# Kernel tuning notes

Hardware: AMD Instinct MI355X
Metric: run time of the kernel (lower is better)

Reference implementation:

```python
import jax, jax.numpy as jnp
import numpy as np

ALPHA = 1.702
LIMIT = 7.0
TOP_K = 2
B, S, H, E, I = 2, 1024, 768, 8, 768


def setup_inputs() -> dict:
    key = jax.random.key(0)
    ks = jax.random.split(key, 7)
    scale = 0.02
    return {
        "hidden_states": jax.random.normal(ks[0], (B, S, H), dtype=jnp.float32),
        "Wr": jax.random.normal(ks[1], (H, E), dtype=jnp.float32) * scale,
        "br": jax.random.normal(ks[2], (E,), dtype=jnp.float32) * scale,
        "Wgu": jax.random.normal(ks[3], (E, H, 2 * I), dtype=jnp.float32) * scale,
        "bgu": jax.random.normal(ks[4], (E, 2 * I), dtype=jnp.float32) * scale,
        "Wd": jax.random.normal(ks[5], (E, I, H), dtype=jnp.float32) * scale,
        "bd": jax.random.normal(ks[6], (E, H), dtype=jnp.float32) * scale,
    }


def reference(hidden_states, Wr, br, Wgu, bgu, Wd, bd):
    # Router: top-K experts per token, softmax over the K selected logits
    logits = jnp.einsum("bsh,he->bse", hidden_states, Wr) + br
    topk_vals, topk_idx = jax.lax.top_k(logits, TOP_K)        # [B,S,K]
    router_scores = jax.nn.softmax(topk_vals, axis=-1)         # [B,S,K]

    # Dense-over-experts grouped GEMM (sparse_matmul reference: unselected
    # experts are computed but never read by the combine gather below).
    gu = jnp.einsum("bsh,ehf->bsef", hidden_states, Wgu) + bgu  # [B,S,E,2I]
    gu = jnp.minimum(gu, LIMIT)
    gate = gu[..., :I]
    up = jnp.maximum(gu[..., I:], -LIMIT)
    glu = gate * jax.nn.sigmoid(gate * ALPHA)
    activated = (up + 1.0) * glu                                # [B,S,E,I]

    down = jnp.einsum("bsei,eih->bseh", activated, Wd) + bd     # [B,S,E,H]

    # all_to_all_combine (num_devices=1): gather this token's K expert outputs
    sel = jnp.take_along_axis(down, topk_idx[..., None], axis=2)  # [B,S,K,H]
    output = jnp.sum(sel * router_scores[..., None], axis=2)      # [B,S,H]
    return output
```

## Files before the change

### kernel.cpp

```cpp
#include <hip/hip_runtime.h>
#include <hip/hip_bf16.h>
#include <cmath>

#define ALPHA 1.702f
#define LIMIT 7.0f

constexpr int B = 2, S = 1024, H = 768, E = 8, I = 768;
constexpr int T = B * S;
constexpr int TWO_I = 2 * I;
constexpr int CAP = T;
constexpr int NROWS = T * 2;

typedef __attribute__((ext_vector_type(8))) short short8;
typedef __attribute__((ext_vector_type(4))) float floatx4;

__device__ __forceinline__ unsigned short f2bf(float v) {
  __hip_bfloat16 h = __float2bfloat16(v);
  return *reinterpret_cast<unsigned short*>(&h);
}

__device__ __forceinline__ void g2l16(const void* g, void* l) {
  __builtin_amdgcn_global_load_lds(
      (const __attribute__((address_space(1))) void*)g,
      (__attribute__((address_space(3))) void*)l, 16, 0, 0);
}

__global__ __launch_bounds__(64) void router_kernel(
    const float* __restrict__ x, const float* __restrict__ Wr,
    const float* __restrict__ br, int* __restrict__ topk_idx,
    float* __restrict__ topk_w, unsigned short* __restrict__ xb,
    float* __restrict__ out) {
  int t = blockIdx.x;
  int lane = threadIdx.x;
  const float* xr = x + (size_t)t * H;

  float4 z4 = {0.f, 0.f, 0.f, 0.f};
#pragma unroll
  for (int j = 0; j < 3; j++)
    *(float4*)(out + (size_t)t * H + (size_t)(j * 64 + lane) * 4) = z4;

  float acc[E];
#pragma unroll
  for (int e = 0; e < E; e++) acc[e] = 0.0f;

#pragma unroll
  for (int it = 0; it < 3; it++) {
    int h4 = it * 64 + lane;
    float4 xv = *(const float4*)(xr + (size_t)h4 * 4);
    ushort4 xo;
    xo.x = f2bf(xv.x);
    xo.y = f2bf(xv.y);
    xo.z = f2bf(xv.z);
    xo.w = f2bf(xv.w);
    *(ushort4*)(xb + (size_t)t * H + (size_t)h4 * 4) = xo;
    const float* wrow = Wr + (size_t)h4 * 4 * E;
    float xs[4] = {xv.x, xv.y, xv.z, xv.w};
#pragma unroll
    for (int j = 0; j < 4; j++)
#pragma unroll
      for (int e = 0; e < E; e++) acc[e] += xs[j] * wrow[j * E + e];
  }
#pragma unroll
  for (int e = 0; e < E; e++) {
    float v = acc[e];
    for (int off = 32; off > 0; off >>= 1) v += __shfl_down(v, off, 64);
    acc[e] = v;
  }
  if (lane == 0) {
    float logits[E];
#pragma unroll
    for (int e = 0; e < E; e++) logits[e] = acc[e] + br[e];
    int i0 = 0;
    float v0 = logits[0];
#pragma unroll
    for (int e = 1; e < E; e++)
      if (logits[e] > v0) { v0 = logits[e]; i0 = e; }
    int i1 = -1;
    float v1 = -INFINITY;
#pragma unroll
    for (int e = 0; e < E; e++) {
      if (e == i0) continue;
      if (logits[e] > v1) { v1 = logits[e]; i1 = e; }
    }
    float s1 = __expf(v1 - v0);
    float denom = 1.0f + s1;
    topk_idx[t * 2 + 0] = i0;
    topk_idx[t * 2 + 1] = i1;
    topk_w[t * 2 + 0] = 1.0f / denom;
    topk_w[t * 2 + 1] = s1 / denom;
  }
}

__global__ __launch_bounds__(256) void transpose_all(
    const float* __restrict__ Wgu, const float* __restrict__ Wd,
    unsigned short* __restrict__ Wgt, unsigned short* __restrict__ Wdt,
    const int* __restrict__ topk_idx, const float* __restrict__ topk_w,
    int* __restrict__ e_cnt, int* __restrict__ row_token,
    float* __restrict__ row_w) {
  int z = blockIdx.z;
  int tid = threadIdx.x;

  if (z == 16) {
    if (blockIdx.x != 0 || blockIdx.y != 0) return;
    __shared__ int cur[E];
    if (tid < E) cur[tid] = 0;
    __syncthreads();
    for (int i = tid; i < NROWS; i += 256) {
      int e = topk_idx[i];
      int pos = atomicAdd(&cur[e], 1);
      row_token[e * CAP + pos] = i >> 1;
      row_w[e * CAP + pos] = topk_w[i];
    }
    __syncthreads();
    if (tid < E) e_cnt[tid] = cur[tid];
    return;
  }

  int which = z >> 3, e = z & 7;
  int N = which ? H : TWO_I;
  if (which && blockIdx.x >= (H / 64)) return;
  const float* in = which ? (Wd + (size_t)e * H * I)
                          : (Wgu + (size_t)e * H * TWO_I);
  unsigned short* out = which ? (Wdt + (size_t)e * H * I)
                              : (Wgt + (size_t)e * H * TWO_I);
  constexpr int K = 768;
  int n0 = blockIdx.x * 64, k0 = blockIdx.y * 64;

  __shared__ float tile[64][65];
  int jr = tid & 15, r0 = tid >> 4;
#pragma unroll
  for (int p = 0; p < 4; p++) {
    int k = r0 + p * 16;
    float4 v = *(const float4*)(in + (size_t)(k0 + k) * N + n0 + jr * 4);
    tile[k][jr * 4 + 0] = v.x;
    tile[k][jr * 4 + 1] = v.y;
    tile[k][jr * 4 + 2] = v.z;
    tile[k][jr * 4 + 3] = v.w;
  }
  __syncthreads();
#pragma unroll
  for (int p = 0; p < 4; p++) {
    int n = r0 + p * 16;
    ushort4 o;
    o.x = f2bf(tile[jr * 4 + 0][n]);
    o.y = f2bf(tile[jr * 4 + 1][n]);
    o.z = f2bf(tile[jr * 4 + 2][n]);
    o.w = f2bf(tile[jr * 4 + 3][n]);
    *(ushort4*)(out + (size_t)(n0 + n) * K + k0 + jr * 4) = o;
  }
}

__global__ __launch_bounds__(256) void gemm_gu_mfma(
    const unsigned short* __restrict__ xb, const unsigned short* __restrict__ Wgt,
    const float* __restrict__ bgu, const int* __restrict__ e_cnt,
    const int* __restrict__ row_token, unsigned short* __restrict__ act) {
  int e = blockIdx.z;
  int cnt = e_cnt[e];
  int m0 = blockIdx.y * 128;
  if (m0 >= cnt) return;
  int n0 = blockIdx.x * 64;
  int start = e * CAP;
  const unsigned short* Wg = Wgt + (size_t)e * TWO_I * H;
  const float* bias = bgu + (size_t)e * TWO_I;

  __shared__ short As[2][128 * 64];
  __shared__ short Bg[2][64 * 64];
  __shared__ short Bu[2][64 * 64];
  __shared__ int tok[128];

  int tid = threadIdx.x;
  if (tid < 128) {
    int m = m0 + tid;
    tok[tid] = row_token[start + ((m < cnt) ? m : (cnt - 1))];
  }
  __syncthreads();

  int lane = tid & 63;
  int wave = tid >> 6;
  int quad = lane >> 4;
  int lrow = lane & 15;
  int wm = (wave >> 1) * 64;
  int wn = (wave & 1) * 32;

  const unsigned short* gA[4];
  int oA[4];
#pragma unroll
  for (int r = 0; r < 4; r++) {
    int s = (wave * 4 + r) * 64 + lane;
    int row = s >> 3;
    int g = (s & 7) ^ (row & 7);
    gA[r] = xb + (size_t)tok[row] * H + g * 8;
    oA[r] = (wave * 4 + r) * 64 * 8;
  }
  const unsigned short *gBg[2], *gBu[2];
  int oB[2];
#pragma unroll
  for (int r = 0; r < 2; r++) {
    int s = (wave * 2 + r) * 64 + lane;
    int row = s >> 3;
    int g = (s & 7) ^ (row & 7);
    gBg[r] = Wg + (size_t)(n0 + row) * H + g * 8;
    gBu[r] = gBg[r] + (size_t)I * H;
    oB[r] = (wave * 2 + r) * 64 * 8;
  }

  float bgv[2], buv[2];
#pragma unroll
  for (int tj = 0; tj < 2; tj++) {
    int ncol = n0 + wn + tj * 16 + lrow;
    bgv[tj] = bias[ncol];
    buv[tj] = bias[I + ncol];
  }

  floatx4 accg[4][2], accu[4][2];
#pragma unroll
  for (int i = 0; i < 4; i++)
#pragma unroll
    for (int j = 0; j < 2; j++) {
      accg[i][j] = floatx4{0.f, 0.f, 0.f, 0.f};
      accu[i][j] = floatx4{0.f, 0.f, 0.f, 0.f};
    }

  __syncthreads();

#pragma unroll
  for (int r = 0; r < 4; r++) g2l16(gA[r], &As[0][oA[r]]);
#pragma unroll
  for (int r = 0; r < 2; r++) {
    g2l16(gBg[r], &Bg[0][oB[r]]);
    g2l16(gBu[r], &Bu[0][oB[r]]);
  }

  constexpr int NK = H / 64;
  for (int i = 0; i < NK; i++) {
    int cb = i & 1;
    if (i + 1 < NK) {
      int nb = cb ^ 1;
      int k1 = (i + 1) * 64;
#pragma unroll
      for (int r = 0; r < 4; r++) g2l16(gA[r] + k1, &As[nb][oA[r]]);
#pragma unroll
      for (int r = 0; r < 2; r++) {
        g2l16(gBg[r] + k1, &Bg[nb][oB[r]]);
        g2l16(gBu[r] + k1, &Bu[nb][oB[r]]);
      }
      asm volatile("s_waitcnt vmcnt(8)" ::: "memory");
    } else {
      asm volatile("s_waitcnt vmcnt(0)" ::: "memory");
    }
    __builtin_amdgcn_s_barrier();

#pragma unroll
    for (int ks = 0; ks < 2; ks++) {
      int c = ks * 4 + quad;
      short8 a[4], bg[2], bu[2];
#pragma unroll
      for (int ti = 0; ti < 4; ti++) {
        int r = wm + ti * 16 + lrow;
        a[ti] = *(const short8*)(&As[cb][(r * 8 + (c ^ (r & 7))) * 8]);
      }
#pragma unroll
      for (int tj = 0; tj < 2; tj++) {
        int r = wn + tj * 16 + lrow;
        bg[tj] = *(const short8*)(&Bg[cb][(r * 8 + (c ^ (r & 7))) * 8]);
        bu[tj] = *(const short8*)(&Bu[cb][(r * 8 + (c ^ (r & 7))) * 8]);
      }
#pragma unroll
      for (int ti = 0; ti < 4; ti++)
#pragma unroll
        for (int tj = 0; tj < 2; tj++) {
          accg[ti][tj] = __builtin_amdgcn_mfma_f32_16x16x32_bf16(
              a[ti], bg[tj], accg[ti][tj], 0, 0, 0);
          accu[ti][tj] = __builtin_amdgcn_mfma_f32_16x16x32_bf16(
              a[ti], bu[tj], accu[ti][tj], 0, 0, 0);
        }
    }
    __builtin_amdgcn_s_barrier();
  }

#pragma unroll
  for (int ti = 0; ti < 4; ti++) {
#pragma unroll
    for (int tj = 0; tj < 2; tj++) {
      int ncol = n0 + wn + tj * 16 + lrow;
#pragma unroll
      for (int r = 0; r < 4; r++) {
        int m = m0 + wm + ti * 16 + quad * 4 + r;
        if (m < cnt) {
          float g = accg[ti][tj][r] + bgv[tj];
          float u = accu[ti][tj][r] + buv[tj];
          g = fminf(g, LIMIT);
          u = fmaxf(fminf(u, LIMIT), -LIMIT);
          float glu = g / (1.0f + __expf(-ALPHA * g));
          act[(size_t)(start + m) * I + ncol] = f2bf((u + 1.0f) * glu);
        }
      }
    }
  }
}

__global__ __launch_bounds__(256) void gemm_down_mfma(
    const unsigned short* __restrict__ act, const unsigned short* __restrict__ Wdt,
    const float* __restrict__ bd, const int* __restrict__ e_cnt,
    const int* __restrict__ row_token, const float* __restrict__ row_w,
    float* __restrict__ out) {
  int e = blockIdx.z;
  int cnt = e_cnt[e];
  int m0 = blockIdx.y * 128;
  if (m0 >= cnt) return;
  int n0 = blockIdx.x * 64;
  int start = e * CAP;
  const unsigned short* Wd = Wdt + (size_t)e * H * I;
  const float* bias = bd + (size_t)e * H;

  __shared__ short As[2][128 * 64];
  __shared__ short Bs[2][64 * 64];
  __shared__ int tok[128];
  __shared__ float wts[128];

  int tid = threadIdx.x;
  if (tid < 128) {
    int m = m0 + tid;
    int mm = (m < cnt) ? m : (cnt - 1);
    tok[tid] = row_token[start + mm];
    wts[tid] = row_w[start + mm];
  }
  __syncthreads();

  int lane = tid & 63;
  int wave = tid >> 6;
  int quad = lane >> 4;
  int lrow = lane & 15;
  int wm = (wave >> 1) * 64;
  int wn = (wave & 1) * 32;

  const unsigned short* gA[4];
  int oA[4];
#pragma unroll
  for (int r = 0; r < 4; r++) {
    int s = (wave * 4 + r) * 64 + lane;
    int row = s >> 3;
    int g = (s & 7) ^ (row & 7);
    int gm = m0 + row;
    int mm = (gm < cnt) ? gm : (cnt - 1);
    gA[r] = act + (size_t)(start + mm) * I + g * 8;
    oA[r] = (wave * 4 + r) * 64 * 8;
  }
  const unsigned short* gB[2];
  int oB[2];
#pragma unroll
  for (int r = 0; r < 2; r++) {
    int s = (wave * 2 + r) * 64 + lane;
    int row = s >> 3;
    int g = (s & 7) ^ (row & 7);
    gB[r] = Wd + (size_t)(n0 + row) * I + g * 8;
    oB[r] = (wave * 2 + r) * 64 * 8;
  }

  float bdv[2];
#pragma unroll
  for (int tj = 0; tj < 2; tj++) bdv[tj] = bias[n0 + wn + tj * 16 + lrow];

  floatx4 acc[4][2];
#pragma unroll
  for (int i = 0; i < 4; i++)
#pragma unroll
    for (int j = 0; j < 2; j++) acc[i][j] = floatx4{0.f, 0.f, 0.f, 0.f};

  __syncthreads();

#pragma unroll
  for (int r = 0; r < 4; r++) g2l16(gA[r], &As[0][oA[r]]);
#pragma unroll
  for (int r = 0; r < 2; r++) g2l16(gB[r], &Bs[0][oB[r]]);

  constexpr int NK = I / 64;
  for (int i = 0; i < NK; i++) {
    int cb = i & 1;
    if (i + 1 < NK) {
      int nb = cb ^ 1;
      int k1 = (i + 1) * 64;
#pragma unroll
      for (int r = 0; r < 4; r++) g2l16(gA[r] + k1, &As[nb][oA[r]]);
#pragma unroll
      for (int r = 0; r < 2; r++) g2l16(gB[r] + k1, &Bs[nb][oB[r]]);
      asm volatile("s_waitcnt vmcnt(6)" ::: "memory");
    } else {
      asm volatile("s_waitcnt vmcnt(0)" ::: "memory");
    }
    __builtin_amdgcn_s_barrier();

#pragma unroll
    for (int ks = 0; ks < 2; ks++) {
      int c = ks * 4 + quad;
      short8 a[4], b[2];
#pragma unroll
      for (int ti = 0; ti < 4; ti++) {
        int r = wm + ti * 16 + lrow;
        a[ti] = *(const short8*)(&As[cb][(r * 8 + (c ^ (r & 7))) * 8]);
      }
#pragma unroll
      for (int tj = 0; tj < 2; tj++) {
        int r = wn + tj * 16 + lrow;
        b[tj] = *(const short8*)(&Bs[cb][(r * 8 + (c ^ (r & 7))) * 8]);
      }
#pragma unroll
      for (int ti = 0; ti < 4; ti++)
#pragma unroll
        for (int tj = 0; tj < 2; tj++)
          acc[ti][tj] = __builtin_amdgcn_mfma_f32_16x16x32_bf16(
              a[ti], b[tj], acc[ti][tj], 0, 0, 0);
    }
    __builtin_amdgcn_s_barrier();
  }

#pragma unroll
  for (int ti = 0; ti < 4; ti++) {
#pragma unroll
    for (int tj = 0; tj < 2; tj++) {
      int ncol = n0 + wn + tj * 16 + lrow;
#pragma unroll
      for (int r = 0; r < 4; r++) {
        int ml = wm + ti * 16 + quad * 4 + r;
        int m = m0 + ml;
        if (m < cnt) {
          atomicAdd(&out[(size_t)tok[ml] * H + ncol],
                    wts[ml] * (acc[ti][tj][r] + bdv[tj]));
        }
      }
    }
  }
}

extern "C" void kernel_launch(void* const* d_in, const int* in_sizes, int n_in,
                              void* d_out, int out_size, void* d_ws,
                              size_t ws_size, hipStream_t stream) {
  const float* x   = (const float*)d_in[0];
  const float* Wr  = (const float*)d_in[1];
  const float* br  = (const float*)d_in[2];
  const float* Wgu = (const float*)d_in[3];
  const float* bgu = (const float*)d_in[4];
  const float* Wd  = (const float*)d_in[5];
  const float* bd  = (const float*)d_in[6];
  float* out = (float*)d_out;

  char* w = (char*)d_ws;
  int* e_cnt = (int*)w;       w += 16 * sizeof(int);
  int* topk_idx = (int*)w;    w += (size_t)T * 2 * sizeof(int);
  float* topk_w = (float*)w;  w += (size_t)T * 2 * sizeof(float);
  int* row_token = (int*)w;   w += (size_t)E * CAP * sizeof(int);
  float* row_w = (float*)w;   w += (size_t)E * CAP * sizeof(float);
  unsigned short* xb  = (unsigned short*)w; w += (size_t)T * H * 2;
  unsigned short* Wgt = (unsigned short*)w; w += (size_t)E * TWO_I * H * 2;
  unsigned short* Wdt = (unsigned short*)w; w += (size_t)E * H * I * 2;
  unsigned short* act = (unsigned short*)w; w += (size_t)E * CAP * I * 2;

  router_kernel<<<T, 64, 0, stream>>>(x, Wr, br, topk_idx, topk_w, xb, out);
  transpose_all<<<dim3(TWO_I / 64, H / 64, 17), 256, 0, stream>>>(
      Wgu, Wd, Wgt, Wdt, topk_idx, topk_w, e_cnt, row_token, row_w);
  gemm_gu_mfma<<<dim3(I / 64, CAP / 128, E), 256, 0, stream>>>(
      xb, Wgt, bgu, e_cnt, row_token, act);
  gemm_down_mfma<<<dim3(H / 64, CAP / 128, E), 256, 0, stream>>>(
      act, Wdt, bd, e_cnt, row_token, row_w, out);
}
```

Before: 171.6 us.

## Load weight tiles directly into registers instead of staging through LDS

Both expert GEMM kernels stop staging the weight (B) tiles in shared memory. Each lane now loads its own MFMA B fragments straight from global memory into double-buffered registers, one k-step ahead, with the k-loop fully unrolled and the vmcnt waits adjusted to match. This shrinks the LDS footprint and removes the LDS reads for B. Launch bounds now request 2 blocks per CU. In exchange, B loads are less coalesced (16-byte per-lane row reads), register pressure rises, and the vmcnt counts must exactly match the reordered loads, or the kernels risk stalls or wrong data.

```diff
diff --git a/kernel.cpp b/kernel.cpp
--- a/kernel.cpp
+++ b/kernel.cpp
@@ -150,7 +150,7 @@
   }
 }
 
-__global__ __launch_bounds__(256) void gemm_gu_mfma(
+__global__ __launch_bounds__(256, 2) void gemm_gu_mfma(
     const unsigned short* __restrict__ xb, const unsigned short* __restrict__ Wgt,
     const float* __restrict__ bgu, const int* __restrict__ e_cnt,
     const int* __restrict__ row_token, unsigned short* __restrict__ act) {
@@ -164,8 +164,6 @@
   const float* bias = bgu + (size_t)e * TWO_I;
 
   __shared__ short As[2][128 * 64];
-  __shared__ short Bg[2][64 * 64];
-  __shared__ short Bu[2][64 * 64];
   __shared__ int tok[128];
 
   int tid = threadIdx.x;
@@ -192,16 +190,13 @@
     gA[r] = xb + (size_t)tok[row] * H + g * 8;
     oA[r] = (wave * 4 + r) * 64 * 8;
   }
-  const unsigned short *gBg[2], *gBu[2];
-  int oB[2];
-#pragma unroll
-  for (int r = 0; r < 2; r++) {
-    int s = (wave * 2 + r) * 64 + lane;
-    int row = s >> 3;
-    int g = (s & 7) ^ (row & 7);
-    gBg[r] = Wg + (size_t)(n0 + row) * H + g * 8;
-    gBu[r] = gBg[r] + (size_t)I * H;
-    oB[r] = (wave * 2 + r) * 64 * 8;
+
+  const unsigned short *bgp[2], *bup[2];
+#pragma unroll
+  for (int tj = 0; tj < 2; tj++) {
+    int n = n0 + wn + tj * 16 + lrow;
+    bgp[tj] = Wg + (size_t)n * H + quad * 8;
+    bup[tj] = bgp[tj] + (size_t)I * H;
   }
 
   float bgv[2], buv[2];
@@ -225,26 +220,32 @@
 
 #pragma unroll
   for (int r = 0; r < 4; r++) g2l16(gA[r], &As[0][oA[r]]);
-#pragma unroll
-  for (int r = 0; r < 2; r++) {
-    g2l16(gBg[r], &Bg[0][oB[r]]);
-    g2l16(gBu[r], &Bu[0][oB[r]]);
-  }
+  short8 bgq[2][2][2], buq[2][2][2];
+#pragma unroll
+  for (int ks = 0; ks < 2; ks++)
+#pragma unroll
+    for (int tj = 0; tj < 2; tj++) {
+      bgq[0][ks][tj] = *(const short8*)(bgp[tj] + ks * 32);
+      buq[0][ks][tj] = *(const short8*)(bup[tj] + ks * 32);
+    }
 
   constexpr int NK = H / 64;
+#pragma unroll
   for (int i = 0; i < NK; i++) {
     int cb = i & 1;
+    int pc = i & 1, pn = pc ^ 1;
     if (i + 1 < NK) {
-      int nb = cb ^ 1;
       int k1 = (i + 1) * 64;
 #pragma unroll
-      for (int r = 0; r < 4; r++) g2l16(gA[r] + k1, &As[nb][oA[r]]);
-#pragma unroll
-      for (int r = 0; r < 2; r++) {
-        g2l16(gBg[r] + k1, &Bg[nb][oB[r]]);
-        g2l16(gBu[r] + k1, &Bu[nb][oB[r]]);
-      }
-      asm volatile("s_waitcnt vmcnt(8)" ::: "memory");
+      for (int r = 0; r < 4; r++) g2l16(gA[r] + k1, &As[cb ^ 1][oA[r]]);
+#pragma unroll
+      for (int ks = 0; ks < 2; ks++)
+#pragma unroll
+        for (int tj = 0; tj < 2; tj++) {
+          bgq[pn][ks][tj] = *(const short8*)(bgp[tj] + k1 + ks * 32);
+          buq[pn][ks][tj] = *(const short8*)(bup[tj] + k1 + ks * 32);
+        }
+      asm volatile("s_waitcnt vmcnt(12)" ::: "memory");
     } else {
       asm volatile("s_waitcnt vmcnt(0)" ::: "memory");
     }
@@ -253,26 +254,20 @@
 #pragma unroll
     for (int ks = 0; ks < 2; ks++) {
       int c = ks * 4 + quad;
-      short8 a[4], bg[2], bu[2];
+      short8 a[4];
 #pragma unroll
       for (int ti = 0; ti < 4; ti++) {
         int r = wm + ti * 16 + lrow;
         a[ti] = *(const short8*)(&As[cb][(r * 8 + (c ^ (r & 7))) * 8]);
       }
 #pragma unroll
-      for (int tj = 0; tj < 2; tj++) {
-        int r = wn + tj * 16 + lrow;
-        bg[tj] = *(const short8*)(&Bg[cb][(r * 8 + (c ^ (r & 7))) * 8]);
-        bu[tj] = *(const short8*)(&Bu[cb][(r * 8 + (c ^ (r & 7))) * 8]);
-      }
-#pragma unroll
       for (int ti = 0; ti < 4; ti++)
 #pragma unroll
         for (int tj = 0; tj < 2; tj++) {
           accg[ti][tj] = __builtin_amdgcn_mfma_f32_16x16x32_bf16(
-              a[ti], bg[tj], accg[ti][tj], 0, 0, 0);
+              a[ti], bgq[pc][ks][tj], accg[ti][tj], 0, 0, 0);
           accu[ti][tj] = __builtin_amdgcn_mfma_f32_16x16x32_bf16(
-              a[ti], bu[tj], accu[ti][tj], 0, 0, 0);
+              a[ti], buq[pc][ks][tj], accu[ti][tj], 0, 0, 0);
         }
     }
     __builtin_amdgcn_s_barrier();
@@ -299,7 +294,7 @@
   }
 }
 
-__global__ __launch_bounds__(256) void gemm_down_mfma(
+__global__ __launch_bounds__(256, 2) void gemm_down_mfma(
     const unsigned short* __restrict__ act, const unsigned short* __restrict__ Wdt,
     const float* __restrict__ bd, const int* __restrict__ e_cnt,
     const int* __restrict__ row_token, const float* __restrict__ row_w,
@@ -314,7 +309,6 @@
   const float* bias = bd + (size_t)e * H;
 
   __shared__ short As[2][128 * 64];
-  __shared__ short Bs[2][64 * 64];
   __shared__ int tok[128];
   __shared__ float wts[128];
 
@@ -346,15 +340,12 @@
     gA[r] = act + (size_t)(start + mm) * I + g * 8;
     oA[r] = (wave * 4 + r) * 64 * 8;
   }
-  const unsigned short* gB[2];
-  int oB[2];
-#pragma unroll
-  for (int r = 0; r < 2; r++) {
-    int s = (wave * 2 + r) * 64 + lane;
-    int row = s >> 3;
-    int g = (s & 7) ^ (row & 7);
-    gB[r] = Wd + (size_t)(n0 + row) * I + g * 8;
-    oB[r] = (wave * 2 + r) * 64 * 8;
+
+  const unsigned short* bp[2];
+#pragma unroll
+  for (int tj = 0; tj < 2; tj++) {
+    int n = n0 + wn + tj * 16 + lrow;
+    bp[tj] = Wd + (size_t)n * I + quad * 8;
   }
 
   float bdv[2];
@@ -371,20 +362,28 @@
 
 #pragma unroll
   for (int r = 0; r < 4; r++) g2l16(gA[r], &As[0][oA[r]]);
-#pragma unroll
-  for (int r = 0; r < 2; r++) g2l16(gB[r], &Bs[0][oB[r]]);
+  short8 bq[2][2][2];
+#pragma unroll
+  for (int ks = 0; ks < 2; ks++)
+#pragma unroll
+    for (int tj = 0; tj < 2; tj++)
+      bq[0][ks][tj] = *(const short8*)(bp[tj] + ks * 32);
 
   constexpr int NK = I / 64;
+#pragma unroll
   for (int i = 0; i < NK; i++) {
     int cb = i & 1;
+    int pc = i & 1, pn = pc ^ 1;
     if (i + 1 < NK) {
-      int nb = cb ^ 1;
       int k1 = (i + 1) * 64;
 #pragma unroll
-      for (int r = 0; r < 4; r++) g2l16(gA[r] + k1, &As[nb][oA[r]]);
-#pragma unroll
-      for (int r = 0; r < 2; r++) g2l16(gB[r] + k1, &Bs[nb][oB[r]]);
-      asm volatile("s_waitcnt vmcnt(6)" ::: "memory");
+      for (int r = 0; r < 4; r++) g2l16(gA[r] + k1, &As[cb ^ 1][oA[r]]);
+#pragma unroll
+      for (int ks = 0; ks < 2; ks++)
+#pragma unroll
+        for (int tj = 0; tj < 2; tj++)
+          bq[pn][ks][tj] = *(const short8*)(bp[tj] + k1 + ks * 32);
+      asm volatile("s_waitcnt vmcnt(8)" ::: "memory");
     } else {
       asm volatile("s_waitcnt vmcnt(0)" ::: "memory");
     }
@@ -393,23 +392,18 @@
 #pragma unroll
     for (int ks = 0; ks < 2; ks++) {
       int c = ks * 4 + quad;
-      short8 a[4], b[2];
+      short8 a[4];
 #pragma unroll
       for (int ti = 0; ti < 4; ti++) {
         int r = wm + ti * 16 + lrow;
         a[ti] = *(const short8*)(&As[cb][(r * 8 + (c ^ (r & 7))) * 8]);
       }
 #pragma unroll
-      for (int tj = 0; tj < 2; tj++) {
-        int r = wn + tj * 16 + lrow;
-        b[tj] = *(const short8*)(&Bs[cb][(r * 8 + (c ^ (r & 7))) * 8]);
-      }
-#pragma unroll
       for (int ti = 0; ti < 4; ti++)
 #pragma unroll
         for (int tj = 0; tj < 2; tj++)
           acc[ti][tj] = __builtin_amdgcn_mfma_f32_16x16x32_bf16(
-              a[ti], b[tj], acc[ti][tj], 0, 0, 0);
+              a[ti], bq[pc][ks][tj], acc[ti][tj], 0, 0, 0);
     }
     __builtin_amdgcn_s_barrier();
   }
```

New measurement: 213.7 us. 24.5% more time.
